# Kernel optimization log

Hardware: AMD Instinct MI355X
Metric: run time of the kernel (lower is better)

## Reference

```python
import jax, jax.numpy as jnp
import numpy as np

B, N, C, H = 8, 2048, 512, 8
D = C // H  # head_dim = 64

def rope(t):
    # t: (B, H, T, D); rotate even/odd interleaved pairs
    T = t.shape[2]
    inv_freq = 1.0 / (10000.0 ** (jnp.arange(0, D, 2, dtype=t.dtype) / D))  # (D/2,)
    pos = jnp.arange(T, dtype=t.dtype)
    freqs = pos[:, None] * inv_freq[None, :]            # (T, D/2)
    cos, sin = jnp.cos(freqs), jnp.sin(freqs)           # broadcast over (B,H)
    t_un = t[..., 0::2]
    t_ev = t[..., 1::2]
    r_un = t_un * cos - t_ev * sin
    r_ev = t_un * sin + t_ev * cos
    # interleave back: (..., D/2, 2) -> (..., D)
    return jnp.stack([r_un, r_ev], axis=-1).reshape(t.shape)

def setup_inputs() -> dict:
    key = jax.random.key(0)
    k1, k2, k3, k4 = jax.random.split(key, 4)
    x = jax.random.normal(k1, (B, N, C), dtype=jnp.float32)
    mask = jax.random.normal(k2, (B, N), dtype=jnp.float32)
    W_qkv = jax.random.normal(k3, (3 * C, C), dtype=jnp.float32) * (1.0 / np.sqrt(C))
    W_proj = jax.random.normal(k4, (C, C), dtype=jnp.float32) * (1.0 / np.sqrt(C))
    b_proj = jnp.zeros((C,), dtype=jnp.float32)
    return {"x": x, "mask": mask, "W_qkv": W_qkv, "W_proj": W_proj,
            "b_proj": b_proj, "num_cls_token": 1}

def reference(x, mask, W_qkv, W_proj, b_proj, num_cls_token):
    scale = D ** (-0.5)
    qkv = jnp.einsum('bnc,fc->bnf', x, W_qkv)             # (B,N,3C)
    qkv = qkv.reshape(B, N, 3, H, D).transpose(2, 0, 3, 1, 4)  # (3,B,H,N,D)
    q, k, v = qkv[0], qkv[1], qkv[2]
    nc = num_cls_token
    if nc > 0:
        q = jnp.concatenate([q[:, :, :nc], rope(q[:, :, nc:])], axis=2)
        k = jnp.concatenate([k[:, :, :nc], rope(k[:, :, nc:])], axis=2)
    else:
        q, k = rope(q), rope(k)
    attn = jnp.einsum('bhnd,bhmd->bhnm', q * scale, k)    # (B,H,N,N)
    attn = attn + mask[:, None, None, :] + mask[:, None, :, None]
    attn = jax.nn.softmax(attn, axis=-1)
    out = jnp.einsum('bhnm,bhmd->bhnd', attn, v)          # (B,H,N,D)
    out = out.transpose(0, 2, 1, 3).reshape(B, N, C)
    return out @ W_proj.T + b_proj
```

## Files before the change

### kernel.cpp

```cpp
#include <hip/hip_runtime.h>
#include <cmath>

#define BB 8
#define NN 2048
#define CC 512
#define HH 8
#define DD 64
#define FF 1536
#define MM (BB*NN)

typedef _Float16 half_t;
typedef __attribute__((ext_vector_type(8))) _Float16 half8;
typedef __attribute__((ext_vector_type(4))) _Float16 half4;
typedef __attribute__((ext_vector_type(2))) __fp16 fp16x2;
typedef __attribute__((ext_vector_type(4))) float floatx4;
typedef __attribute__((ext_vector_type(16))) float floatx16;
typedef __attribute__((ext_vector_type(4))) float fx4;

#define LOG2E 1.44269504088896f
#define EXP2_OFF 4.3280851f

typedef const __attribute__((address_space(1))) unsigned int* gas_ptr;
typedef __attribute__((address_space(3))) unsigned int* las_ptr;
__device__ __forceinline__ void gld16(const half_t* g, half_t* l) {
  __builtin_amdgcn_global_load_lds((gas_ptr)g, (las_ptr)l, 16, 0, 0);
}

#define N1 (MM * CC / 8)
#define N2 (FF * CC / 8)
#define N3 (CC * CC / 8)
#define NC (N1 + N2 + N3)
#define NR (NN * 32)
#define NPREP (NC + NR + MM)
__global__ __launch_bounds__(256) void prep_kernel(
    const float* __restrict__ x, const float* __restrict__ wq,
    const float* __restrict__ wp, const float* __restrict__ mask,
    half_t* __restrict__ d, float2* __restrict__ tab, float* __restrict__ msb) {
  int i = blockIdx.x * 256 + threadIdx.x;
  if (i < NC) {
    const float* s;
    if (i < N1)            s = x  + (size_t)i * 8;
    else if (i < N1 + N2)  s = wq + (size_t)(i - N1) * 8;
    else                   s = wp + (size_t)(i - N1 - N2) * 8;
    float4 a = ((const float4*)s)[0], b = ((const float4*)s)[1];
    half8 h;
    h[0] = (half_t)a.x; h[1] = (half_t)a.y; h[2] = (half_t)a.z; h[3] = (half_t)a.w;
    h[4] = (half_t)b.x; h[5] = (half_t)b.y; h[6] = (half_t)b.z; h[7] = (half_t)b.w;
    ((half8*)d)[i] = h;
  } else if (i < NC + NR) {
    int e = i - NC;
    int p = e >> 5, j = e & 31;
    float ang = (float)p * __powf(10000.0f, -(float)(2 * j) * (1.0f / 64.0f));
    float sv, cv;
    __sincosf(ang, &sv, &cv);
    tab[e] = make_float2(cv, sv);
  } else {
    int k = i - NC - NR;
    msb[k] = mask[k] * LOG2E - EXP2_OFF;
  }
}

__global__ __launch_bounds__(256, 4) void qkv_mfma_kernel(
    const half_t* __restrict__ Ah,
    const half_t* __restrict__ Bh,
    const int*   __restrict__ ncp,
    const float2* __restrict__ tab,
    half_t* __restrict__ Qh, half_t* __restrict__ Kh, half_t* __restrict__ Vt)
{
  __shared__ union {
    struct { half_t A[2][128 * 32]; half_t B[2][128 * 32]; } s;
    half_t T[4][64 * 68];
  } sm;

  const int tid  = threadIdx.x;
  const int wave = tid >> 6, lane = tid & 63;
  const int L15  = lane & 15, quad = lane >> 4;
  const int wm = (wave & 1) * 64, wn = (wave >> 1) * 64;
  const int m0 = blockIdx.x * 128;
  const int f0 = blockIdx.y * 128;

  const int srow = lane >> 2;
  const int scolh = (lane & 3) * 8;
  const half_t* Ag = Ah + (size_t)(m0 + wave * 16 + srow) * CC + scolh;
  const half_t* Bg = Bh + (size_t)(f0 + wave * 16 + srow) * CC + scolh;

  floatx4 acc[4][4];
#pragma unroll
  for (int i = 0; i < 4; ++i)
#pragma unroll
    for (int j = 0; j < 4; ++j) acc[i][j] = (floatx4){0.f, 0.f, 0.f, 0.f};

#define QSTAGE(c, koff)                                                       \
  {                                                                           \
    gld16(Ag + (koff),           &sm.s.A[c][(wave * 16) * 32]);               \
    gld16(Ag + (koff) + 64 * CC, &sm.s.A[c][(64 + wave * 16) * 32]);          \
    gld16(Bg + (koff),           &sm.s.B[c][(wave * 16) * 32]);               \
    gld16(Bg + (koff) + 64 * CC, &sm.s.B[c][(64 + wave * 16) * 32]);          \
  }

#define QCOMPUTE(c)                                                           \
  {                                                                           \
    half8 af[4], bf[4];                                                       \
    _Pragma("unroll")                                                         \
    for (int mi = 0; mi < 4; ++mi)                                            \
      af[mi] = *(const half8*)&sm.s.A[c][(wm + mi * 16 + L15) * 32 + quad * 8]; \
    _Pragma("unroll")                                                         \
    for (int ni = 0; ni < 4; ++ni)                                            \
      bf[ni] = *(const half8*)&sm.s.B[c][(wn + ni * 16 + L15) * 32 + quad * 8]; \
    __builtin_amdgcn_s_setprio(1);                                            \
    _Pragma("unroll")                                                         \
    for (int mi = 0; mi < 4; ++mi)                                            \
      _Pragma("unroll")                                                       \
      for (int ni = 0; ni < 4; ++ni)                                          \
        acc[mi][ni] = __builtin_amdgcn_mfma_f32_16x16x32_f16(bf[ni], af[mi], acc[mi][ni], 0, 0, 0); \
    __builtin_amdgcn_s_setprio(0);                                            \
  }

  QSTAGE(0, 0)
  QSTAGE(1, 32)
  asm volatile("s_waitcnt vmcnt(4)");
  __builtin_amdgcn_s_barrier();
  __builtin_amdgcn_sched_barrier(0);

  int k0 = 64;
#pragma unroll 1
  for (int kk = 0; kk < 7; ++kk) {
    QCOMPUTE(0)
    __builtin_amdgcn_sched_barrier(0);
    __builtin_amdgcn_s_barrier();
    QSTAGE(0, k0)
    asm volatile("s_waitcnt vmcnt(4)");
    __builtin_amdgcn_s_barrier();
    __builtin_amdgcn_sched_barrier(0);

    QCOMPUTE(1)
    __builtin_amdgcn_sched_barrier(0);
    __builtin_amdgcn_s_barrier();
    QSTAGE(1, k0 + 32)
    asm volatile("s_waitcnt vmcnt(4)");
    __builtin_amdgcn_s_barrier();
    __builtin_amdgcn_sched_barrier(0);
    k0 += 64;
  }
  QCOMPUTE(0)
  asm volatile("s_waitcnt vmcnt(0)");
  __builtin_amdgcn_s_barrier();
  __builtin_amdgcn_sched_barrier(0);
  QCOMPUTE(1)

#undef QSTAGE
#undef QCOMPUTE

  const int which = f0 >> 9;
  const int b     = m0 >> 11;
  const int n_base = (m0 & 2047) + wm;
  const int h     = ((f0 + wn) >> 6) & 7;

  if (which < 2) {
    const int nc = *ncp;
    half_t* dst = which ? Kh : Qh;
    const float qscale = which ? 1.0f : (0.125f * LOG2E);
    const float* tabf = (const float*)tab;
#pragma unroll
    for (int mi = 0; mi < 4; ++mi) {
      const int n = n_base + mi * 16 + L15;
      const int p = n - nc;
      const size_t rbase = (((size_t)(b * HH + h) * NN + n) << 6) + quad * 4;
#pragma unroll
      for (int ni = 0; ni < 4; ++ni) {
        float o0 = acc[mi][ni][0], o1 = acc[mi][ni][1];
        float o2 = acc[mi][ni][2], o3 = acc[mi][ni][3];
        if (p >= 0) {
          const fx4 c4 = *(const fx4*)(tabf + p * 64 + ni * 16 + quad * 4);
          const float e0 = o0, e1 = o1, e2 = o2, e3 = o3;
          o0 = e0 * c4[0] - e1 * c4[1];
          o1 = e0 * c4[1] + e1 * c4[0];
          o2 = e2 * c4[2] - e3 * c4[3];
          o3 = e2 * c4[3] + e3 * c4[2];
        }
        half4 hv;
        hv[0] = (half_t)(o0 * qscale); hv[1] = (half_t)(o1 * qscale);
        hv[2] = (half_t)(o2 * qscale); hv[3] = (half_t)(o3 * qscale);
        *(half4*)(dst + rbase + ni * 16) = hv;
      }
    }
  } else {
    __syncthreads();
#pragma unroll
    for (int ni = 0; ni < 4; ++ni)
#pragma unroll
      for (int mi = 0; mi < 4; ++mi)
#pragma unroll
        for (int r = 0; r < 4; ++r)
          sm.T[wave][(ni * 16 + quad * 4 + r) * 68 + mi * 16 + L15] = (half_t)acc[mi][ni][r];
    __syncthreads();
    const size_t gbase = ((size_t)(b * HH + h) * DD + lane) * NN + n_base;
#pragma unroll
    for (int c = 0; c < 8; ++c)
      *(half8*)(Vt + gbase + c * 8) = *(const half8*)&sm.T[wave][lane * 68 + c * 8];
  }
}

__global__ __launch_bounds__(256, 4) void flash_mfma_kernel(
    const half_t* __restrict__ Qh,
    const half_t* __restrict__ Kh,
    const half_t* __restrict__ Vt,
    const float*  __restrict__ ms,
    half_t* __restrict__ O)
{
  __shared__ half_t KV[2][2][64 * 64];
  __shared__ __align__(16) float Ms[2048];

  const int tid  = threadIdx.x;
  const int wave = tid >> 6;
  const int lane = tid & 63;
  const int l31  = lane & 31;
  const int hi   = lane >> 5;
  const int l7   = lane & 7;

  const int bid  = blockIdx.x;
  const int xcd  = bid & 7;
  const int slot = bid >> 3;
  const int qt   = slot & 15;
  const int head = (slot >> 4) * 8 + xcd;
  const int b    = head >> 3;
  const int h    = head & 7;

  const half_t* Kt_base = Kh + ((((size_t)b * HH + h) * NN) << 6);
  const half_t* Vt_base = Vt + (((size_t)b * HH + h) * DD) * NN;

  half8 qf[4];
  {
    const half_t* Qp =
        Qh + ((((size_t)b * HH + h) * NN + qt * 128 + wave * 32 + l31) << 6) + hi * 8;
#pragma unroll
    for (int kd = 0; kd < 4; ++kd) qf[kd] = *(const half8*)(Qp + kd * 16);
  }

  const int r8  = lane >> 3;
  const int dof = ((l7 ^ r8) << 3);
  const half_t* kbase = Kt_base + (((size_t)(wave * 16 + r8)) << 6) + dof;
  const half_t* vbase = Vt_base + (size_t)(wave * 16 + r8) * NN + dof;

  int adK[4], adV[4];
#pragma unroll
  for (int c = 0; c < 4; ++c) {
    adK[c] = l31 * 128 + ((((c << 1) | hi) ^ l7) << 4);
    adV[c] = 8192 + l31 * 128 + ((((c << 1) | hi) ^ l7) << 4);
  }
  const char* L = (const char*)KV;

  floatx16 acc[2];
#pragma unroll
  for (int dt = 0; dt < 2; ++dt)
#pragma unroll
    for (int r = 0; r < 16; ++r) acc[dt][r] = 0.f;
  float l4[4] = {0.f, 0.f, 0.f, 0.f};

#define STAGE(c, koff, voff)                                                  \
  {                                                                           \
    gld16(kbase + (koff),          &KV[c][0][wave * 1024]);                   \
    gld16(kbase + (koff) + 512,    &KV[c][0][wave * 1024 + 512]);             \
    gld16(vbase + (voff),          &KV[c][1][wave * 1024]);                   \
    gld16(vbase + (voff) + 8 * NN, &KV[c][1][wave * 1024 + 512]);             \
  }

#define COMPUTE(c, moffB)                                                     \
  _Pragma("unroll")                                                           \
  for (int t = 0; t < 2; ++t) {                                               \
    floatx16 S;                                                               \
    _Pragma("unroll")                                                         \
    for (int r2 = 0; r2 < 4; ++r2) {                                          \
      fx4 mv = *(const fx4*)((const char*)Ms + mls + (moffB) + t * 128 + r2 * 32); \
      S[r2 * 4 + 0] = mv[0]; S[r2 * 4 + 1] = mv[1];                           \
      S[r2 * 4 + 2] = mv[2]; S[r2 * 4 + 3] = mv[3];                           \
    }                                                                         \
    __builtin_amdgcn_s_setprio(1);                                            \
    _Pragma("unroll")                                                         \
    for (int kd = 0; kd < 4; ++kd) {                                          \
      half8 kf = *(const half8*)(L + (adK[kd] + (c) * 16384 + t * 4096));     \
      S = __builtin_amdgcn_mfma_f32_32x32x16_f16(kf, qf[kd], S, 0, 0, 0);     \
    }                                                                         \
    __builtin_amdgcn_s_setprio(0);                                            \
    _Pragma("unroll")                                                         \
    for (int r = 0; r < 16; ++r) {                                            \
      float p = __builtin_amdgcn_exp2f(S[r]);                                 \
      l4[r & 3] += p;                                                         \
      S[r] = p;                                                               \
    }                                                                         \
    unsigned W[4][2];                                                         \
    _Pragma("unroll")                                                         \
    for (int r2 = 0; r2 < 4; ++r2)                                            \
      _Pragma("unroll")                                                       \
      for (int u = 0; u < 2; ++u) {                                           \
        union { fp16x2 h; unsigned w; } pk;                                   \
        pk.h = __builtin_amdgcn_cvt_pkrtz(S[r2 * 4 + 2 * u],                  \
                                          S[r2 * 4 + 2 * u + 1]);             \
        W[r2][u] = pk.w;                                                      \
      }                                                                       \
    _Pragma("unroll")                                                         \
    for (int ksl = 0; ksl < 2; ++ksl) {                                       \
      unsigned A0 = W[2 * ksl][0],     A1 = W[2 * ksl][1];                    \
      unsigned B0 = W[2 * ksl + 1][0], B1 = W[2 * ksl + 1][1];                \
      asm("v_permlane32_swap_b32 %0, %1" : "+v"(A0), "+v"(B0));               \
      asm("v_permlane32_swap_b32 %0, %1" : "+v"(A1), "+v"(B1));               \
      union { unsigned u4[4]; half8 v; } pw;                                  \
      pw.u4[0] = A0; pw.u4[1] = A1; pw.u4[2] = B0; pw.u4[3] = B1;             \
      const int ks = t * 2 + ksl;                                             \
      __builtin_amdgcn_s_setprio(1);                                          \
      _Pragma("unroll")                                                       \
      for (int dt = 0; dt < 2; ++dt) {                                        \
        half8 vf = *(const half8*)(L + (adV[ks] + (c) * 16384 + dt * 4096));  \
        acc[dt] = __builtin_amdgcn_mfma_f32_32x32x16_f16(pw.v, vf, acc[dt], 0, 0, 0); \
      }                                                                       \
      __builtin_amdgcn_s_setprio(0);                                          \
    }                                                                         \
  }

  STAGE(0, 0, 0)
  {
    const half_t* msrc = (const half_t*)(ms + (size_t)b * NN + wave * 512 + lane * 4);
    gld16(msrc,                    (half_t*)Ms + wave * 1024);
    gld16(msrc + 512,              (half_t*)Ms + wave * 1024 + 512);
  }
  STAGE(1, 4096, 64)
  asm volatile("s_waitcnt vmcnt(4)");
  __builtin_amdgcn_s_barrier();
  __builtin_amdgcn_sched_barrier(0);
  kbase += 8192; vbase += 128;

  int mls = hi * 16;
#pragma unroll 1
  for (int kt2 = 0; kt2 < 15; ++kt2) {
    COMPUTE(0, 0)
    __builtin_amdgcn_sched_barrier(0);
    __builtin_amdgcn_s_barrier();
    STAGE(0, 0, 0)
    asm volatile("s_waitcnt vmcnt(4)");
    __builtin_amdgcn_s_barrier();
    __builtin_amdgcn_sched_barrier(0);

    COMPUTE(1, 256)
    __builtin_amdgcn_sched_barrier(0);
    __builtin_amdgcn_s_barrier();
    STAGE(1, 4096, 64)
    asm volatile("s_waitcnt vmcnt(4)");
    __builtin_amdgcn_s_barrier();
    __builtin_amdgcn_sched_barrier(0);

    kbase += 8192; vbase += 128;
    mls += 512;
  }

  COMPUTE(0, 0)
  asm volatile("s_waitcnt vmcnt(0)");
  __builtin_amdgcn_s_barrier();
  __builtin_amdgcn_sched_barrier(0);
  COMPUTE(1, 256)

#undef STAGE
#undef COMPUTE

  float l_part = (l4[0] + l4[1]) + (l4[2] + l4[3]);
  l_part += __shfl_xor(l_part, 32, 64);

  const size_t orow = (size_t)b * NN + qt * 128 + wave * 32;
#pragma unroll
  for (int r = 0; r < 16; ++r) {
    const int ql  = (r & 3) + 8 * (r >> 2) + 4 * hi;
    const float iv = 1.0f / __shfl(l_part, ql, 64);
    const size_t ro = ((orow + ql) << 9) + (h << 6) + l31;
    O[ro]      = (half_t)(acc[0][r] * iv);
    O[ro + 32] = (half_t)(acc[1][r] * iv);
  }
}

__global__ __launch_bounds__(256) void proj_mfma_kernel(
    const half_t* __restrict__ Ah,
    const half_t* __restrict__ Bh,
    const float* __restrict__ bias,
    float* __restrict__ out)
{
  __shared__ half_t As[2][128 * 32];
  __shared__ half_t Bs[2][64 * 32];

  const int tid  = threadIdx.x;
  const int wave = tid >> 6, lane = tid & 63;
  const int L15  = lane & 15, quad = lane >> 4;
  const int wm = (wave & 1) * 64, wn = (wave >> 1) * 32;
  const int m0 = blockIdx.x * 128;
  const int f0 = blockIdx.y * 64;

  const int srow = lane >> 2;
  const int scolh = (lane & 3) * 8;
  const half_t* Ag = Ah + (size_t)(m0 + wave * 16 + srow) * CC + scolh;
  const half_t* Bg = Bh + (size_t)(f0 + wave * 16 + srow) * CC + scolh;

  floatx4 acc[4][2];
#pragma unroll
  for (int i = 0; i < 4; ++i)
#pragma unroll
    for (int j = 0; j < 2; ++j) acc[i][j] = (floatx4){0.f, 0.f, 0.f, 0.f};

#define PSTAGE(c, koff)                                                       \
  {                                                                           \
    gld16(Ag + (koff),           &As[c][(wave * 16) * 32]);                   \
    gld16(Ag + (koff) + 64 * CC, &As[c][(64 + wave * 16) * 32]);              \
    gld16(Bg + (koff),           &Bs[c][(wave * 16) * 32]);                   \
  }

#define PCOMPUTE(c)                                                           \
  {                                                                           \
    half8 af[4], bf[2];                                                       \
    _Pragma("unroll")                                                         \
    for (int mi = 0; mi < 4; ++mi)                                            \
      af[mi] = *(const half8*)&As[c][(wm + mi * 16 + L15) * 32 + quad * 8];   \
    _Pragma("unroll")                                                         \
    for (int ni = 0; ni < 2; ++ni)                                            \
      bf[ni] = *(const half8*)&Bs[c][(wn + ni * 16 + L15) * 32 + quad * 8];   \
    __builtin_amdgcn_s_setprio(1);                                            \
    _Pragma("unroll")                                                         \
    for (int mi = 0; mi < 4; ++mi)                                            \
      _Pragma("unroll")                                                       \
      for (int ni = 0; ni < 2; ++ni)                                          \
        acc[mi][ni] = __builtin_amdgcn_mfma_f32_16x16x32_f16(af[mi], bf[ni], acc[mi][ni], 0, 0, 0); \
    __builtin_amdgcn_s_setprio(0);                                            \
  }

  PSTAGE(0, 0)
  PSTAGE(1, 32)
  asm volatile("s_waitcnt vmcnt(3)");
  __builtin_amdgcn_s_barrier();
  __builtin_amdgcn_sched_barrier(0);

  int k0 = 64;
#pragma unroll 1
  for (int kk = 0; kk < 7; ++kk) {
    PCOMPUTE(0)
    __builtin_amdgcn_sched_barrier(0);
    __builtin_amdgcn_s_barrier();
    PSTAGE(0, k0)
    asm volatile("s_waitcnt vmcnt(3)");
    __builtin_amdgcn_s_barrier();
    __builtin_amdgcn_sched_barrier(0);

    PCOMPUTE(1)
    __builtin_amdgcn_sched_barrier(0);
    __builtin_amdgcn_s_barrier();
    PSTAGE(1, k0 + 32)
    asm volatile("s_waitcnt vmcnt(3)");
    __builtin_amdgcn_s_barrier();
    __builtin_amdgcn_sched_barrier(0);
    k0 += 64;
  }
  PCOMPUTE(0)
  asm volatile("s_waitcnt vmcnt(0)");
  __builtin_amdgcn_s_barrier();
  __builtin_amdgcn_sched_barrier(0);
  PCOMPUTE(1)

#undef PSTAGE
#undef PCOMPUTE

#pragma unroll
  for (int ni = 0; ni < 2; ++ni) {
    const int f = f0 + wn + ni * 16 + L15;
    const float bv = bias[f];
#pragma unroll
    for (int mi = 0; mi < 4; ++mi)
#pragma unroll
      for (int r = 0; r < 4; ++r)
        out[(size_t)(m0 + wm + mi * 16 + quad * 4 + r) * CC + f] = acc[mi][ni][r] + bv;
  }
}

extern "C" void kernel_launch(void* const* d_in, const int* in_sizes, int n_in,
                              void* d_out, int out_size, void* d_ws, size_t ws_size,
                              hipStream_t stream) {
  const float* x     = (const float*)d_in[0];
  const float* mask  = (const float*)d_in[1];
  const float* Wqkv  = (const float*)d_in[2];
  const float* Wproj = (const float*)d_in[3];
  const float* bproj = (const float*)d_in[4];
  const int*   ncp   = (const int*)d_in[5];
  float* out = (float*)d_out;

  const size_t per = (size_t)BB * HH * NN * DD;
  half_t* xh  = (half_t*)d_ws;
  half_t* Wqh = xh + (size_t)MM * CC;
  half_t* Wph = Wqh + (size_t)FF * CC;
  half_t* Qh  = Wph + (size_t)CC * CC;
  half_t* Kh  = Qh + per;
  half_t* Vt  = Kh + per;
  half_t* Oh  = Vt + per;
  float2* tab = (float2*)(Oh + per);
  float*  msb = (float*)(tab + (size_t)NN * 32);

  prep_kernel<<<dim3(NPREP / 256), 256, 0, stream>>>(x, Wqkv, Wproj, mask, xh, tab, msb);

  qkv_mfma_kernel<<<dim3(MM / 128, FF / 128), 256, 0, stream>>>(xh, Wqh, ncp, tab, Qh, Kh, Vt);
  flash_mfma_kernel<<<dim3(BB * HH * (NN / 128)), 256, 0, stream>>>(Qh, Kh, Vt, msb, Oh);
  proj_mfma_kernel<<<dim3(MM / 128, CC / 64), 256, 0, stream>>>(Oh, Wph, bproj, out);
}
```

Measured before the change: 231.7 us.

## Process two 32-row query blocks per wave in flash kernel with 2-wave blocks

The flash attention kernel now uses 2 waves per block instead of 4, with each wave computing two 32-row query sub-tiles. Each K/V fragment read from LDS is reused for twice as many MFMAs. Each wave also stages twice as much K/V and mask data, so the vmcnt waits change accordingly. This cuts LDS read traffic and barrier participants per unit of work, at the cost of more registers per wave (two score tiles and four accumulators) and fewer waves in flight.

Result: no change. 231.6 us (-0.0%).

```diff
diff --git a/kernel.cpp b/kernel.cpp
--- a/kernel.cpp
+++ b/kernel.cpp
@@ -201,7 +201,7 @@
   }
 }
 
-__global__ __launch_bounds__(256, 4) void flash_mfma_kernel(
+__global__ __launch_bounds__(128, 2) void flash_mfma_kernel(
     const half_t* __restrict__ Qh,
     const half_t* __restrict__ Kh,
     const half_t* __restrict__ Vt,
@@ -229,18 +229,21 @@
   const half_t* Kt_base = Kh + ((((size_t)b * HH + h) * NN) << 6);
   const half_t* Vt_base = Vt + (((size_t)b * HH + h) * DD) * NN;
 
-  half8 qf[4];
+  half8 qf0[4], qf1[4];
   {
-    const half_t* Qp =
-        Qh + ((((size_t)b * HH + h) * NN + qt * 128 + wave * 32 + l31) << 6) + hi * 8;
-#pragma unroll
-    for (int kd = 0; kd < 4; ++kd) qf[kd] = *(const half8*)(Qp + kd * 16);
+    const half_t* Qp0 =
+        Qh + ((((size_t)b * HH + h) * NN + qt * 128 + wave * 64 + l31) << 6) + hi * 8;
+#pragma unroll
+    for (int kd = 0; kd < 4; ++kd) {
+      qf0[kd] = *(const half8*)(Qp0 + kd * 16);
+      qf1[kd] = *(const half8*)(Qp0 + 32 * 64 + kd * 16);
+    }
   }
 
   const int r8  = lane >> 3;
   const int dof = ((l7 ^ r8) << 3);
-  const half_t* kbase = Kt_base + (((size_t)(wave * 16 + r8)) << 6) + dof;
-  const half_t* vbase = Vt_base + (size_t)(wave * 16 + r8) * NN + dof;
+  const half_t* kbase = Kt_base + (((size_t)(wave * 32 + r8)) << 6) + dof;
+  const half_t* vbase = Vt_base + (size_t)(wave * 32 + r8) * NN + dof;
 
   int adK[4], adV[4];
 #pragma unroll
@@ -250,68 +253,88 @@
   }
   const char* L = (const char*)KV;
 
-  floatx16 acc[2];
-#pragma unroll
-  for (int dt = 0; dt < 2; ++dt)
-#pragma unroll
-    for (int r = 0; r < 16; ++r) acc[dt][r] = 0.f;
-  float l4[4] = {0.f, 0.f, 0.f, 0.f};
+  floatx16 acc[2][2];
+#pragma unroll
+  for (int qb = 0; qb < 2; ++qb)
+#pragma unroll
+    for (int dt = 0; dt < 2; ++dt)
+#pragma unroll
+      for (int r = 0; r < 16; ++r) acc[qb][dt][r] = 0.f;
+  float l4[2][4] = {{0.f, 0.f, 0.f, 0.f}, {0.f, 0.f, 0.f, 0.f}};
 
 #define STAGE(c, koff, voff)                                                  \
   {                                                                           \
-    gld16(kbase + (koff),          &KV[c][0][wave * 1024]);                   \
-    gld16(kbase + (koff) + 512,    &KV[c][0][wave * 1024 + 512]);             \
-    gld16(vbase + (voff),          &KV[c][1][wave * 1024]);                   \
-    gld16(vbase + (voff) + 8 * NN, &KV[c][1][wave * 1024 + 512]);             \
+    gld16(kbase + (koff),           &KV[c][0][wave * 2048]);                  \
+    gld16(kbase + (koff) + 512,     &KV[c][0][wave * 2048 + 512]);            \
+    gld16(kbase + (koff) + 1024,    &KV[c][0][wave * 2048 + 1024]);           \
+    gld16(kbase + (koff) + 1536,    &KV[c][0][wave * 2048 + 1536]);           \
+    gld16(vbase + (voff),           &KV[c][1][wave * 2048]);                  \
+    gld16(vbase + (voff) + 8 * NN,  &KV[c][1][wave * 2048 + 512]);            \
+    gld16(vbase + (voff) + 16 * NN, &KV[c][1][wave * 2048 + 1024]);           \
+    gld16(vbase + (voff) + 24 * NN, &KV[c][1][wave * 2048 + 1536]);           \
   }
 
 #define COMPUTE(c, moffB)                                                     \
   _Pragma("unroll")                                                           \
   for (int t = 0; t < 2; ++t) {                                               \
-    floatx16 S;                                                               \
+    floatx16 S0, S1;                                                          \
     _Pragma("unroll")                                                         \
     for (int r2 = 0; r2 < 4; ++r2) {                                          \
       fx4 mv = *(const fx4*)((const char*)Ms + mls + (moffB) + t * 128 + r2 * 32); \
-      S[r2 * 4 + 0] = mv[0]; S[r2 * 4 + 1] = mv[1];                           \
-      S[r2 * 4 + 2] = mv[2]; S[r2 * 4 + 3] = mv[3];                           \
+      S0[r2 * 4 + 0] = mv[0]; S0[r2 * 4 + 1] = mv[1];                         \
+      S0[r2 * 4 + 2] = mv[2]; S0[r2 * 4 + 3] = mv[3];                         \
+      S1[r2 * 4 + 0] = mv[0]; S1[r2 * 4 + 1] = mv[1];                         \
+      S1[r2 * 4 + 2] = mv[2]; S1[r2 * 4 + 3] = mv[3];                         \
     }                                                                         \
     __builtin_amdgcn_s_setprio(1);                                            \
     _Pragma("unroll")                                                         \
     for (int kd = 0; kd < 4; ++kd) {                                          \
       half8 kf = *(const half8*)(L + (adK[kd] + (c) * 16384 + t * 4096));     \
-      S = __builtin_amdgcn_mfma_f32_32x32x16_f16(kf, qf[kd], S, 0, 0, 0);     \
+      S0 = __builtin_amdgcn_mfma_f32_32x32x16_f16(kf, qf0[kd], S0, 0, 0, 0);  \
+      S1 = __builtin_amdgcn_mfma_f32_32x32x16_f16(kf, qf1[kd], S1, 0, 0, 0);  \
     }                                                                         \
     __builtin_amdgcn_s_setprio(0);                                            \
     _Pragma("unroll")                                                         \
     for (int r = 0; r < 16; ++r) {                                            \
-      float p = __builtin_amdgcn_exp2f(S[r]);                                 \
-      l4[r & 3] += p;                                                         \
-      S[r] = p;                                                               \
+      float p0 = __builtin_amdgcn_exp2f(S0[r]);                               \
+      l4[0][r & 3] += p0;  S0[r] = p0;                                        \
+      float p1 = __builtin_amdgcn_exp2f(S1[r]);                               \
+      l4[1][r & 3] += p1;  S1[r] = p1;                                        \
     }                                                                         \
-    unsigned W[4][2];                                                         \
+    unsigned W0[4][2], W1[4][2];                                              \
     _Pragma("unroll")                                                         \
     for (int r2 = 0; r2 < 4; ++r2)                                            \
       _Pragma("unroll")                                                       \
       for (int u = 0; u < 2; ++u) {                                           \
         union { fp16x2 h; unsigned w; } pk;                                   \
-        pk.h = __builtin_amdgcn_cvt_pkrtz(S[r2 * 4 + 2 * u],                  \
-                                          S[r2 * 4 + 2 * u + 1]);             \
-        W[r2][u] = pk.w;                                                      \
+        pk.h = __builtin_amdgcn_cvt_pkrtz(S0[r2 * 4 + 2 * u],                 \
+                                          S0[r2 * 4 + 2 * u + 1]);            \
+        W0[r2][u] = pk.w;                                                     \
+        pk.h = __builtin_amdgcn_cvt_pkrtz(S1[r2 * 4 + 2 * u],                 \
+                                          S1[r2 * 4 + 2 * u + 1]);            \
+        W1[r2][u] = pk.w;                                                     \
       }                                                                       \
     _Pragma("unroll")                                                         \
     for (int ksl = 0; ksl < 2; ++ksl) {                                       \
-      unsigned A0 = W[2 * ksl][0],     A1 = W[2 * ksl][1];                    \
-      unsigned B0 = W[2 * ksl + 1][0], B1 = W[2 * ksl + 1][1];                \
+      unsigned A0 = W0[2 * ksl][0],     A1 = W0[2 * ksl][1];                  \
+      unsigned B0 = W0[2 * ksl + 1][0], B1 = W0[2 * ksl + 1][1];              \
       asm("v_permlane32_swap_b32 %0, %1" : "+v"(A0), "+v"(B0));               \
       asm("v_permlane32_swap_b32 %0, %1" : "+v"(A1), "+v"(B1));               \
-      union { unsigned u4[4]; half8 v; } pw;                                  \
-      pw.u4[0] = A0; pw.u4[1] = A1; pw.u4[2] = B0; pw.u4[3] = B1;             \
+      union { unsigned u4[4]; half8 v; } pw0;                                 \
+      pw0.u4[0] = A0; pw0.u4[1] = A1; pw0.u4[2] = B0; pw0.u4[3] = B1;         \
+      unsigned C0 = W1[2 * ksl][0],     C1 = W1[2 * ksl][1];                  \
+      unsigned D0 = W1[2 * ksl + 1][0], D1 = W1[2 * ksl + 1][1];              \
+      asm("v_permlane32_swap_b32 %0, %1" : "+v"(C0), "+v"(D0));               \
+      asm("v_permlane32_swap_b32 %0, %1" : "+v"(C1), "+v"(D1));               \
+      union { unsigned u4[4]; half8 v; } pw1;                                 \
+      pw1.u4[0] = C0; pw1.u4[1] = C1; pw1.u4[2] = D0; pw1.u4[3] = D1;         \
       const int ks = t * 2 + ksl;                                             \
       __builtin_amdgcn_s_setprio(1);                                          \
       _Pragma("unroll")                                                       \
       for (int dt = 0; dt < 2; ++dt) {                                        \
         half8 vf = *(const half8*)(L + (adV[ks] + (c) * 16384 + dt * 4096));  \
-        acc[dt] = __builtin_amdgcn_mfma_f32_32x32x16_f16(pw.v, vf, acc[dt], 0, 0, 0); \
+        acc[0][dt] = __builtin_amdgcn_mfma_f32_32x32x16_f16(pw0.v, vf, acc[0][dt], 0, 0, 0); \
+        acc[1][dt] = __builtin_amdgcn_mfma_f32_32x32x16_f16(pw1.v, vf, acc[1][dt], 0, 0, 0); \
       }                                                                       \
       __builtin_amdgcn_s_setprio(0);                                          \
     }                                                                         \
@@ -319,12 +342,14 @@
 
   STAGE(0, 0, 0)
   {
-    const half_t* msrc = (const half_t*)(ms + (size_t)b * NN + wave * 512 + lane * 4);
-    gld16(msrc,                    (half_t*)Ms + wave * 1024);
-    gld16(msrc + 512,              (half_t*)Ms + wave * 1024 + 512);
+    const half_t* msrc = (const half_t*)(ms + (size_t)b * NN) + wave * 2048 + lane * 8;
+    gld16(msrc,        (half_t*)Ms + wave * 2048);
+    gld16(msrc + 512,  (half_t*)Ms + wave * 2048 + 512);
+    gld16(msrc + 1024, (half_t*)Ms + wave * 2048 + 1024);
+    gld16(msrc + 1536, (half_t*)Ms + wave * 2048 + 1536);
   }
   STAGE(1, 4096, 64)
-  asm volatile("s_waitcnt vmcnt(4)");
+  asm volatile("s_waitcnt vmcnt(8)");
   __builtin_amdgcn_s_barrier();
   __builtin_amdgcn_sched_barrier(0);
   kbase += 8192; vbase += 128;
@@ -336,7 +361,7 @@
     __builtin_amdgcn_sched_barrier(0);
     __builtin_amdgcn_s_barrier();
     STAGE(0, 0, 0)
-    asm volatile("s_waitcnt vmcnt(4)");
+    asm volatile("s_waitcnt vmcnt(8)");
     __builtin_amdgcn_s_barrier();
     __builtin_amdgcn_sched_barrier(0);
 
@@ -344,7 +369,7 @@
     __builtin_amdgcn_sched_barrier(0);
     __builtin_amdgcn_s_barrier();
     STAGE(1, 4096, 64)
-    asm volatile("s_waitcnt vmcnt(4)");
+    asm volatile("s_waitcnt vmcnt(8)");
     __builtin_amdgcn_s_barrier();
     __builtin_amdgcn_sched_barrier(0);
 
@@ -361,17 +386,19 @@
 #undef STAGE
 #undef COMPUTE
 
-  float l_part = (l4[0] + l4[1]) + (l4[2] + l4[3]);
-  l_part += __shfl_xor(l_part, 32, 64);
-
-  const size_t orow = (size_t)b * NN + qt * 128 + wave * 32;
-#pragma unroll
-  for (int r = 0; r < 16; ++r) {
-    const int ql  = (r & 3) + 8 * (r >> 2) + 4 * hi;
-    const float iv = 1.0f / __shfl(l_part, ql, 64);
-    const size_t ro = ((orow + ql) << 9) + (h << 6) + l31;
-    O[ro]      = (half_t)(acc[0][r] * iv);
-    O[ro + 32] = (half_t)(acc[1][r] * iv);
+#pragma unroll
+  for (int qb = 0; qb < 2; ++qb) {
+    float l_part = (l4[qb][0] + l4[qb][1]) + (l4[qb][2] + l4[qb][3]);
+    l_part += __shfl_xor(l_part, 32, 64);
+    const size_t orow = (size_t)b * NN + qt * 128 + wave * 64 + qb * 32;
+#pragma unroll
+    for (int r = 0; r < 16; ++r) {
+      const int ql  = (r & 3) + 8 * (r >> 2) + 4 * hi;
+      const float iv = 1.0f / __shfl(l_part, ql, 64);
+      const size_t ro = ((orow + ql) << 9) + (h << 6) + l31;
+      O[ro]      = (half_t)(acc[qb][0][r] * iv);
+      O[ro + 32] = (half_t)(acc[qb][1][r] * iv);
+    }
   }
 }
 
@@ -499,6 +526,6 @@
   prep_kernel<<<dim3(NPREP / 256), 256, 0, stream>>>(x, Wqkv, Wproj, mask, xh, tab, msb);
 
   qkv_mfma_kernel<<<dim3(MM / 128, FF / 128), 256, 0, stream>>>(xh, Wqh, ncp, tab, Qh, Kh, Vt);
-  flash_mfma_kernel<<<dim3(BB * HH * (NN / 128)), 256, 0, stream>>>(Qh, Kh, Vt, msb, Oh);
+  flash_mfma_kernel<<<dim3(BB * HH * (NN / 128)), 128, 0, stream>>>(Qh, Kh, Vt, msb, Oh);
   proj_mfma_kernel<<<dim3(MM / 128, CC / 64), 256, 0, stream>>>(Oh, Wph, bproj, out);
 }
```
